# Performance work log

Hardware: AMD Instinct MI355X
Metric: run time of the kernel (lower is better)

## Reference

```python
import jax, jax.numpy as jnp
import numpy as np

B = 16
S_IN, S_DIM, Z_DIM, PE_DIM = 21, 256, 64, 64
REGIONS = ["cdr3", "pep", "mhc", "hv", "hj", "lv", "lj"]
LENS = {"cdr3": 24, "pep": 16, "mhc": 48, "hv": 104, "hj": 16, "lv": 104, "lj": 14}
L_TOTAL = 1 + sum(LENS.values())  # 327 = collapse token + all regions (full masks)
N_COND = 6


def _pos_enc(L):
    # sinusoidal PE matching one_d_positional_encoding: sin for even i, cos for odd i,
    # both with divisor 10000**(i/dim)
    pos = jnp.arange(L, dtype=jnp.float32)
    i = jnp.arange(PE_DIM)
    ang = pos[:, None] / (10000.0 ** (i.astype(jnp.float32) / PE_DIM))
    return jnp.where(i % 2 == 0, jnp.sin(ang), jnp.cos(ang))  # [L, 64]


def _pair_id():
    # region label per position: 0=psi, 1=cdr3, 2..7 = conditioning regions in order
    reg = np.concatenate([[0]] + [[k + 1] * LENS[r] for k, r in enumerate(REGIONS)])
    reg = jnp.asarray(reg, dtype=jnp.int32)
    ri, rj = reg[:, None], reg[None, :]
    i = jnp.arange(L_TOTAL, dtype=jnp.int32)[:, None]
    j = jnp.arange(L_TOTAL, dtype=jnp.int32)[None, :]
    p = jnp.zeros((L_TOTAL, L_TOTAL), dtype=jnp.int32)
    p = jnp.where((i == 0) | (j == 0), 1, p)                    # lvl1: psi <-> all
    p = jnp.where((i == 0) & (j == 0), 0, p)                    # lvl0: psi self
    cb = (ri == 1) & (rj == 1)
    p = jnp.where(cb & (jnp.abs(i - j) == 1), 2, p)             # lvl2: cdr3 sequential
    p = jnp.where(cb & (i != j) & (jnp.abs(i - j) != 1), 3, p)  # lvl3: cdr3 internal
    p = jnp.where(((ri == 1) & (rj >= 2)) | ((ri >= 2) & (rj == 1)), 4, p)  # lvl4
    p = jnp.where((ri >= 2) & (ri == rj), 5 + (ri - 2), p)      # lvl5..10: cond internal
    a = jnp.minimum(ri, rj) - 2
    b = jnp.maximum(ri, rj) - 2
    cross = a * (2 * N_COND - a - 1) // 2 + (b - a - 1)         # upper-tri pair index
    p = jnp.where((ri >= 2) & (rj >= 2) & (ri != rj), 11 + cross, p)  # lvl11..25
    return jnp.minimum(p, 31)


def _region_emb(seq, w2, seq_W, seq_b, pos_W, pos_b):
    # seq: [B, Lr, 21] -> [B, Lr, 256]
    se = jnp.einsum('bld,ed->ble', seq, seq_W) + seq_b
    pe = _pos_enc(seq.shape[1]) @ pos_W.T + pos_b  # [Lr, 256]
    return w2[0] * se + w2[1] * pe


def setup_inputs() -> dict:
    key = jax.random.key(0)
    ks = jax.random.split(key, 16)
    inp = {}
    for n, (name, r) in enumerate(zip(
            ['cdr3_xt', 'pep_seq', 'mhc_seq', 'hv_seq', 'hj_seq', 'lv_seq', 'lj_seq'], REGIONS)):
        inp[name] = jax.random.normal(ks[n], (B, LENS[r], S_IN), dtype=jnp.float32)
    inp['seq_W'] = jax.random.normal(ks[7], (S_DIM, S_IN), dtype=jnp.float32) * 0.1
    inp['seq_b'] = jnp.zeros((S_DIM,), dtype=jnp.float32)
    inp['pos_W'] = jax.random.normal(ks[8], (S_DIM, PE_DIM), dtype=jnp.float32) * 0.1
    inp['pos_b'] = jnp.zeros((S_DIM,), dtype=jnp.float32)
    inp['pair1_W'] = jax.random.normal(ks[9], (Z_DIM // 2, 8), dtype=jnp.float32) * 0.3
    inp['pair1_b'] = jnp.zeros((Z_DIM // 2,), dtype=jnp.float32)
    inp['pair2_W'] = jax.random.normal(ks[10], (Z_DIM // 2, 4), dtype=jnp.float32) * 0.3
    inp['pair2_b'] = jnp.zeros((Z_DIM // 2,), dtype=jnp.float32)
    inp['collapse_token'] = jax.random.normal(ks[11], (1, S_DIM), dtype=jnp.float32) * 0.1
    inp['collapse_weight'] = jnp.ones((1,), dtype=jnp.float32)
    inp['region_w'] = jax.random.uniform(ks[12], (7, 2), dtype=jnp.float32) + 0.5
    for name, r in zip(['cdr3_mask', 'pep_mask', 'mhc_mask', 'hv_mask', 'hj_mask', 'lv_mask', 'lj_mask'], REGIONS):
        inp[name] = jnp.ones((B, LENS[r]), dtype=jnp.int32)
    return inp


def reference(cdr3_xt, pep_seq, mhc_seq, hv_seq, hj_seq, lv_seq, lj_seq,
              seq_W, seq_b, pos_W, pos_b, pair1_W, pair1_b, pair2_W, pair2_b,
              collapse_token, collapse_weight, region_w,
              cdr3_mask, pep_mask, mhc_mask, hv_mask, hj_mask, lv_mask, lj_mask):
    # masks are all-ones -> every region is full-length (static shapes); they are
    # only used in torch to derive lengths, so they are closed-over constants here.
    seqs = [cdr3_xt, pep_seq, mhc_seq, hv_seq, hj_seq, lv_seq, lj_seq]
    parts = [jnp.broadcast_to(collapse_weight * collapse_token, (B, 1, S_DIM))]
    for k, seq in enumerate(seqs):
        parts.append(_region_emb(seq, region_w[k], seq_W, seq_b, pos_W, pos_b))
    s = jnp.concatenate(parts, axis=1)  # [B, 327, 256]
    p = _pair_id()                      # [327, 327] int32, identical across batch
    # one_hot(k, n) @ W.T + b  ==  (W.T + b)[k]  -> pure gather from tiny tables
    t1 = pair1_W.T + pair1_b            # [8, 32]
    t2 = pair2_W.T + pair2_b            # [4, 32]
    z = jnp.concatenate([t1[p // 4], t2[p % 4]], axis=-1)        # [327, 327, 64]
    z = jnp.broadcast_to(z[None], (B, L_TOTAL, L_TOTAL, Z_DIM))  # per-sample z list -> stacked
    return s, z
```

## Files before the change

kernel.cpp:

```cpp
#include <hip/hip_runtime.h>
#include <math.h>

#define NB 16
#define LTOT 327
#define SDIM 256
#define ZD 64

__device__ __constant__ int d_starts[7] = {1, 25, 41, 89, 193, 209, 313};
__device__ __constant__ int d_lens[7]   = {24, 16, 48, 104, 16, 104, 14};

__device__ __constant__ int seg_s[8] = {0, 1, 25, 41, 89, 193, 209, 313};
__device__ __constant__ int seg_e[8] = {1, 25, 41, 89, 193, 209, 313, 327};

__device__ __forceinline__ int regid(int x) {
    return (x >= 1) + (x >= 25) + (x >= 41) + (x >= 89) + (x >= 193) + (x >= 209) + (x >= 313);
}

__device__ __forceinline__ int pair_id(int i, int j, int ri, int rj) {
    if ((i == 0) && (j == 0)) return 0;
    if ((i == 0) || (j == 0)) return 1;
    if ((ri == 1) && (rj == 1)) {
        int d = i > j ? i - j : j - i;
        if (d == 1) return 2;
        if (d != 0) return 3;
        return 0;
    }
    if ((ri == 1) || (rj == 1)) return 4;
    if (ri == rj) return 5 + ri - 2;
    int a = (ri < rj ? ri : rj) - 2;
    int c = (ri < rj ? rj : ri) - 2;
    return 11 + a * (11 - a) / 2 + (c - a - 1);
}

__global__ __launch_bounds__(256) void pe_kernel(
    const float* __restrict__ posW, const float* __restrict__ posb,
    const float* __restrict__ rw, float* __restrict__ pe_full)
{
    int l = blockIdx.x;
    int e = threadIdx.x;
    __shared__ float sh_pe[64];

    int k = (l >= 25) + (l >= 41) + (l >= 89) + (l >= 193) + (l >= 209) + (l >= 313);
    int pl = (l == 0) ? 0 : (l - d_starts[k]);
    if (e < 64) {
        float scale = exp2f(-(float)e * (13.287712379549449f / 64.0f));
        float ang = (float)pl * scale;
        sh_pe[e] = (e & 1) ? cosf(ang) : sinf(ang);
    }
    __syncthreads();

    float pe = posb[e];
    const float* pwrow = posW + e * 64;
    #pragma unroll 8
    for (int i2 = 0; i2 < 64; i2++) pe = fmaf(sh_pe[i2], pwrow[i2], pe);
    pe_full[(size_t)l * SDIM + e] = rw[2 * k + 1] * pe;
}

__global__ __launch_bounds__(256) void s_kernel2(
    const float* __restrict__ s0, const float* __restrict__ s1,
    const float* __restrict__ s2, const float* __restrict__ s3,
    const float* __restrict__ s4, const float* __restrict__ s5,
    const float* __restrict__ s6,
    const float* __restrict__ seqW, const float* __restrict__ seqb,
    const float* __restrict__ ctok, const float* __restrict__ cw,
    const float* __restrict__ rw, const float* __restrict__ pe_full,
    float* __restrict__ out)
{
    int blk = blockIdx.x;
    int l = blk % LTOT;
    int b = blk / LTOT;
    int e = threadIdx.x;

    if (l == 0) {
        out[(size_t)blk * SDIM + e] = cw[0] * ctok[e];
        return;
    }
    __shared__ float sh_seq[21];
    int k = (l >= 25) + (l >= 41) + (l >= 89) + (l >= 193) + (l >= 209) + (l >= 313);
    int pl = l - d_starts[k];
    const float* sp;
    switch (k) {
        case 0: sp = s0; break; case 1: sp = s1; break; case 2: sp = s2; break;
        case 3: sp = s3; break; case 4: sp = s4; break; case 5: sp = s5; break;
        default: sp = s6;
    }
    if (e < 21) sh_seq[e] = sp[((size_t)b * d_lens[k] + pl) * 21 + e];
    __syncthreads();

    float se = seqb[e];
    const float* wrow = seqW + e * 21;
    #pragma unroll
    for (int d = 0; d < 21; d++) se = fmaf(sh_seq[d], wrow[d], se);

    out[(size_t)blk * SDIM + e] = rw[2 * k] * se + pe_full[(size_t)l * SDIM + e];
}

__global__ __launch_bounds__(256) void s_kernel(
    const float* __restrict__ s0, const float* __restrict__ s1,
    const float* __restrict__ s2, const float* __restrict__ s3,
    const float* __restrict__ s4, const float* __restrict__ s5,
    const float* __restrict__ s6,
    const float* __restrict__ seqW, const float* __restrict__ seqb,
    const float* __restrict__ posW, const float* __restrict__ posb,
    const float* __restrict__ ctok, const float* __restrict__ cw,
    const float* __restrict__ rw,
    float* __restrict__ out)
{
    int blk = blockIdx.x;
    int l = blk % LTOT;
    int b = blk / LTOT;
    int e = threadIdx.x;
    if (l == 0) { out[(size_t)blk * SDIM + e] = cw[0] * ctok[e]; return; }
    __shared__ float sh_seq[21];
    __shared__ float sh_pe[64];
    int k = (l >= 25) + (l >= 41) + (l >= 89) + (l >= 193) + (l >= 209) + (l >= 313);
    int pl = l - d_starts[k];
    const float* sp;
    switch (k) {
        case 0: sp = s0; break; case 1: sp = s1; break; case 2: sp = s2; break;
        case 3: sp = s3; break; case 4: sp = s4; break; case 5: sp = s5; break;
        default: sp = s6;
    }
    if (e < 21) sh_seq[e] = sp[((size_t)b * d_lens[k] + pl) * 21 + e];
    if (e < 64) {
        float scale = exp2f(-(float)e * (13.287712379549449f / 64.0f));
        float ang = (float)pl * scale;
        sh_pe[e] = (e & 1) ? cosf(ang) : sinf(ang);
    }
    __syncthreads();
    float se = seqb[e];
    const float* wrow = seqW + e * 21;
    #pragma unroll
    for (int d = 0; d < 21; d++) se = fmaf(sh_seq[d], wrow[d], se);
    float pe = posb[e];
    const float* pwrow = posW + e * 64;
    #pragma unroll 8
    for (int i2 = 0; i2 < 64; i2++) pe = fmaf(sh_pe[i2], pwrow[i2], pe);
    out[(size_t)blk * SDIM + e] = rw[2 * k] * se + rw[2 * k + 1] * pe;
}

#define TSTRIDE 68

__global__ __launch_bounds__(256) void z_kernel(
    const float* __restrict__ p1W, const float* __restrict__ p1b,
    const float* __restrict__ p2W, const float* __restrict__ p2b,
    float* __restrict__ outz)
{
    __shared__ __align__(16) float table[32 * TSTRIDE];
    int t = threadIdx.x;

    for (int idx = t; idx < 32 * 64; idx += 256) {
        int p = idx >> 6, c = idx & 63;
        float v;
        if (c < 32) v = p1W[c * 8 + (p >> 2)] + p1b[c];
        else        v = p2W[(c - 32) * 4 + (p & 3)] + p2b[c - 32];
        table[p * TSTRIDE + c] = v;
    }
    __syncthreads();

    int blk = blockIdx.x;
    int i = blk % LTOT;
    int ri = regid(i);
    int c4 = t & 15;
    int jo = t >> 4;

    float4* dst = (float4*)(outz + (size_t)blk * (LTOT * ZD));

    #pragma unroll
    for (int s = 0; s < 8; s++) {
        int js = seg_s[s], je = seg_e[s];
        if (ri == 1 && s == 1) {
            float4 v0 = *(const float4*)(table + 0 * TSTRIDE + c4 * 4);
            float4 v2 = *(const float4*)(table + 2 * TSTRIDE + c4 * 4);
            float4 v3 = *(const float4*)(table + 3 * TSTRIDE + c4 * 4);
            for (int j = js + jo; j < je; j += 16) {
                int d = i > j ? i - j : j - i;
                float4 v = (d == 0) ? v0 : ((d == 1) ? v2 : v3);
                dst[j * 16 + c4] = v;
            }
        } else {
            int p = pair_id(i, js, ri, regid(js));
            float4 v = *(const float4*)(table + p * TSTRIDE + c4 * 4);
            for (int j = js + jo; j < je; j += 16) {
                dst[j * 16 + c4] = v;
            }
        }
    }
}

extern "C" void kernel_launch(void* const* d_in, const int* in_sizes, int n_in,
                              void* d_out, int out_size, void* d_ws, size_t ws_size,
                              hipStream_t stream) {
    const float* seq0 = (const float*)d_in[0];
    const float* seq1 = (const float*)d_in[1];
    const float* seq2 = (const float*)d_in[2];
    const float* seq3 = (const float*)d_in[3];
    const float* seq4 = (const float*)d_in[4];
    const float* seq5 = (const float*)d_in[5];
    const float* seq6 = (const float*)d_in[6];
    const float* seqW = (const float*)d_in[7];
    const float* seqb = (const float*)d_in[8];
    const float* posW = (const float*)d_in[9];
    const float* posb = (const float*)d_in[10];
    const float* p1W  = (const float*)d_in[11];
    const float* p1b  = (const float*)d_in[12];
    const float* p2W  = (const float*)d_in[13];
    const float* p2b  = (const float*)d_in[14];
    const float* ctok = (const float*)d_in[15];
    const float* cw   = (const float*)d_in[16];
    const float* rw   = (const float*)d_in[17];

    float* out = (float*)d_out;
    float* outz = out + (size_t)NB * LTOT * SDIM;

    z_kernel<<<NB * LTOT, 256, 0, stream>>>(p1W, p1b, p2W, p2b, outz);

    if (ws_size >= (size_t)LTOT * SDIM * sizeof(float)) {
        float* pe_full = (float*)d_ws;
        pe_kernel<<<LTOT, 256, 0, stream>>>(posW, posb, rw, pe_full);
        s_kernel2<<<NB * LTOT, 256, 0, stream>>>(seq0, seq1, seq2, seq3, seq4, seq5, seq6,
                                                 seqW, seqb, ctok, cw, rw, pe_full, out);
    } else {
        s_kernel<<<NB * LTOT, 256, 0, stream>>>(seq0, seq1, seq2, seq3, seq4, seq5, seq6,
                                                seqW, seqb, posW, posb, ctok, cw, rw, out);
    }
}
```

Measured before the change: 507.1 us.

## Fuse z and s kernels into one launch with nontemporal 32-byte stores

Merges the z pair-table broadcast kernel and the s embedding kernel into one launch, with the block index choosing which branch runs. The z stores become nontemporal, and each thread writes two 16-byte vectors (32 bytes) per row. The s path now stages seqW in shared memory. The aim is to cut a launch, let the small s work overlap the bandwidth-bound z writes, and keep the z output from polluting cache. The cost is a larger shared allocation for every block, which may lower occupancy for the z blocks.

```diff
diff --git a/kernel.cpp b/kernel.cpp
--- a/kernel.cpp
+++ b/kernel.cpp
@@ -5,6 +5,9 @@
 #define LTOT 327
 #define SDIM 256
 #define ZD 64
+#define NZ (NB * LTOT)
+
+typedef float nt4 __attribute__((ext_vector_type(4)));
 
 __device__ __constant__ int d_starts[7] = {1, 25, 41, 89, 193, 209, 313};
 __device__ __constant__ int d_lens[7]   = {24, 16, 48, 104, 16, 104, 14};
@@ -56,7 +59,11 @@
     pe_full[(size_t)l * SDIM + e] = rw[2 * k + 1] * pe;
 }
 
-__global__ __launch_bounds__(256) void s_kernel2(
+#define TSTRIDE 68
+
+__global__ __launch_bounds__(256) void fused_zs(
+    const float* __restrict__ p1W, const float* __restrict__ p1b,
+    const float* __restrict__ p2W, const float* __restrict__ p2b,
     const float* __restrict__ s0, const float* __restrict__ s1,
     const float* __restrict__ s2, const float* __restrict__ s3,
     const float* __restrict__ s4, const float* __restrict__ s5,
@@ -64,82 +71,93 @@
     const float* __restrict__ seqW, const float* __restrict__ seqb,
     const float* __restrict__ ctok, const float* __restrict__ cw,
     const float* __restrict__ rw, const float* __restrict__ pe_full,
-    float* __restrict__ out)
-{
+    float* __restrict__ out, float* __restrict__ outz)
+{
+    __shared__ __align__(16) float smem[5408];
+    int t = threadIdx.x;
     int blk = blockIdx.x;
-    int l = blk % LTOT;
-    int b = blk / LTOT;
-    int e = threadIdx.x;
-
-    if (l == 0) {
-        out[(size_t)blk * SDIM + e] = cw[0] * ctok[e];
-        return;
-    }
-    __shared__ float sh_seq[21];
-    int k = (l >= 25) + (l >= 41) + (l >= 89) + (l >= 193) + (l >= 209) + (l >= 313);
-    int pl = l - d_starts[k];
-    const float* sp;
-    switch (k) {
-        case 0: sp = s0; break; case 1: sp = s1; break; case 2: sp = s2; break;
-        case 3: sp = s3; break; case 4: sp = s4; break; case 5: sp = s5; break;
-        default: sp = s6;
-    }
-    if (e < 21) sh_seq[e] = sp[((size_t)b * d_lens[k] + pl) * 21 + e];
-    __syncthreads();
-
-    float se = seqb[e];
-    const float* wrow = seqW + e * 21;
-    #pragma unroll
-    for (int d = 0; d < 21; d++) se = fmaf(sh_seq[d], wrow[d], se);
-
-    out[(size_t)blk * SDIM + e] = rw[2 * k] * se + pe_full[(size_t)l * SDIM + e];
-}
-
-__global__ __launch_bounds__(256) void s_kernel(
-    const float* __restrict__ s0, const float* __restrict__ s1,
-    const float* __restrict__ s2, const float* __restrict__ s3,
-    const float* __restrict__ s4, const float* __restrict__ s5,
-    const float* __restrict__ s6,
-    const float* __restrict__ seqW, const float* __restrict__ seqb,
-    const float* __restrict__ posW, const float* __restrict__ posb,
-    const float* __restrict__ ctok, const float* __restrict__ cw,
-    const float* __restrict__ rw,
-    float* __restrict__ out)
-{
-    int blk = blockIdx.x;
-    int l = blk % LTOT;
-    int b = blk / LTOT;
-    int e = threadIdx.x;
-    if (l == 0) { out[(size_t)blk * SDIM + e] = cw[0] * ctok[e]; return; }
-    __shared__ float sh_seq[21];
-    __shared__ float sh_pe[64];
-    int k = (l >= 25) + (l >= 41) + (l >= 89) + (l >= 193) + (l >= 209) + (l >= 313);
-    int pl = l - d_starts[k];
-    const float* sp;
-    switch (k) {
-        case 0: sp = s0; break; case 1: sp = s1; break; case 2: sp = s2; break;
-        case 3: sp = s3; break; case 4: sp = s4; break; case 5: sp = s5; break;
-        default: sp = s6;
-    }
-    if (e < 21) sh_seq[e] = sp[((size_t)b * d_lens[k] + pl) * 21 + e];
-    if (e < 64) {
-        float scale = exp2f(-(float)e * (13.287712379549449f / 64.0f));
-        float ang = (float)pl * scale;
-        sh_pe[e] = (e & 1) ? cosf(ang) : sinf(ang);
-    }
-    __syncthreads();
-    float se = seqb[e];
-    const float* wrow = seqW + e * 21;
-    #pragma unroll
-    for (int d = 0; d < 21; d++) se = fmaf(sh_seq[d], wrow[d], se);
-    float pe = posb[e];
-    const float* pwrow = posW + e * 64;
-    #pragma unroll 8
-    for (int i2 = 0; i2 < 64; i2++) pe = fmaf(sh_pe[i2], pwrow[i2], pe);
-    out[(size_t)blk * SDIM + e] = rw[2 * k] * se + rw[2 * k + 1] * pe;
-}
-
-#define TSTRIDE 68
+
+    if (blk < NZ) {
+        float* table = smem;
+        for (int idx = t; idx < 32 * 64; idx += 256) {
+            int p = idx >> 6, c = idx & 63;
+            float v;
+            if (c < 32) v = p1W[c * 8 + (p >> 2)] + p1b[c];
+            else        v = p2W[(c - 32) * 4 + (p & 3)] + p2b[c - 32];
+            table[p * TSTRIDE + c] = v;
+        }
+        __syncthreads();
+
+        int i = blk % LTOT;
+        int ri = regid(i);
+        int c8 = t & 7;
+        int jo = t >> 3;
+
+        nt4* dst = (nt4*)(outz + (size_t)blk * (LTOT * ZD)) + c8 * 2;
+
+        #pragma unroll
+        for (int s = 0; s < 8; s++) {
+            int js = seg_s[s], je = seg_e[s];
+            if (ri == 1 && s == 1) {
+                const nt4* r0 = (const nt4*)(table + 0 * TSTRIDE) + c8 * 2;
+                const nt4* r2 = (const nt4*)(table + 2 * TSTRIDE) + c8 * 2;
+                const nt4* r3 = (const nt4*)(table + 3 * TSTRIDE) + c8 * 2;
+                nt4 v0a = r0[0], v0b = r0[1];
+                nt4 v2a = r2[0], v2b = r2[1];
+                nt4 v3a = r3[0], v3b = r3[1];
+                for (int j = js + jo; j < je; j += 32) {
+                    int d = i > j ? i - j : j - i;
+                    nt4 va = (d == 0) ? v0a : ((d == 1) ? v2a : v3a);
+                    nt4 vb = (d == 0) ? v0b : ((d == 1) ? v2b : v3b);
+                    __builtin_nontemporal_store(va, dst + j * 16);
+                    __builtin_nontemporal_store(vb, dst + j * 16 + 1);
+                }
+            } else {
+                int p = pair_id(i, js, ri, regid(js));
+                const nt4* rp = (const nt4*)(table + p * TSTRIDE) + c8 * 2;
+                nt4 va = rp[0], vb = rp[1];
+                for (int j = js + jo; j < je; j += 32) {
+                    __builtin_nontemporal_store(va, dst + j * 16);
+                    __builtin_nontemporal_store(vb, dst + j * 16 + 1);
+                }
+            }
+        }
+    } else {
+        int sb = blk - NZ;
+        int l = sb % LTOT;
+        int b = sb / LTOT;
+        int e = t;
+
+        if (l == 0) {
+            out[(size_t)sb * SDIM + e] = cw[0] * ctok[e];
+            return;
+        }
+        float* sh_w   = smem;
+        float* sh_seq = smem + 5376;
+
+        const float4* wsrc = (const float4*)seqW;
+        float4* wdst = (float4*)sh_w;
+        for (int idx = t; idx < 1344; idx += 256) wdst[idx] = wsrc[idx];
+
+        int k = (l >= 25) + (l >= 41) + (l >= 89) + (l >= 193) + (l >= 209) + (l >= 313);
+        int pl = l - d_starts[k];
+        const float* sp;
+        switch (k) {
+            case 0: sp = s0; break; case 1: sp = s1; break; case 2: sp = s2; break;
+            case 3: sp = s3; break; case 4: sp = s4; break; case 5: sp = s5; break;
+            default: sp = s6;
+        }
+        if (e < 21) sh_seq[e] = sp[((size_t)b * d_lens[k] + pl) * 21 + e];
+        __syncthreads();
+
+        float se = seqb[e];
+        const float* wrow = sh_w + e * 21;
+        #pragma unroll
+        for (int d = 0; d < 21; d++) se = fmaf(sh_seq[d], wrow[d], se);
+
+        out[(size_t)sb * SDIM + e] = rw[2 * k] * se + pe_full[(size_t)l * SDIM + e];
+    }
+}
 
 __global__ __launch_bounds__(256) void z_kernel(
     const float* __restrict__ p1W, const float* __restrict__ p1b,
@@ -148,7 +166,6 @@
 {
     __shared__ __align__(16) float table[32 * TSTRIDE];
     int t = threadIdx.x;
-
     for (int idx = t; idx < 32 * 64; idx += 256) {
         int p = idx >> 6, c = idx & 63;
         float v;
@@ -163,7 +180,6 @@
     int ri = regid(i);
     int c4 = t & 15;
     int jo = t >> 4;
-
     float4* dst = (float4*)(outz + (size_t)blk * (LTOT * ZD));
 
     #pragma unroll
@@ -186,6 +202,50 @@
             }
         }
     }
+}
+
+__global__ __launch_bounds__(256) void s_kernel(
+    const float* __restrict__ s0, const float* __restrict__ s1,
+    const float* __restrict__ s2, const float* __restrict__ s3,
+    const float* __restrict__ s4, const float* __restrict__ s5,
+    const float* __restrict__ s6,
+    const float* __restrict__ seqW, const float* __restrict__ seqb,
+    const float* __restrict__ posW, const float* __restrict__ posb,
+    const float* __restrict__ ctok, const float* __restrict__ cw,
+    const float* __restrict__ rw,
+    float* __restrict__ out)
+{
+    int blk = blockIdx.x;
+    int l = blk % LTOT;
+    int b = blk / LTOT;
+    int e = threadIdx.x;
+    if (l == 0) { out[(size_t)blk * SDIM + e] = cw[0] * ctok[e]; return; }
+    __shared__ float sh_seq[21];
+    __shared__ float sh_pe[64];
+    int k = (l >= 25) + (l >= 41) + (l >= 89) + (l >= 193) + (l >= 209) + (l >= 313);
+    int pl = l - d_starts[k];
+    const float* sp;
+    switch (k) {
+        case 0: sp = s0; break; case 1: sp = s1; break; case 2: sp = s2; break;
+        case 3: sp = s3; break; case 4: sp = s4; break; case 5: sp = s5; break;
+        default: sp = s6;
+    }
+    if (e < 21) sh_seq[e] = sp[((size_t)b * d_lens[k] + pl) * 21 + e];
+    if (e < 64) {
+        float scale = exp2f(-(float)e * (13.287712379549449f / 64.0f));
+        float ang = (float)pl * scale;
+        sh_pe[e] = (e & 1) ? cosf(ang) : sinf(ang);
+    }
+    __syncthreads();
+    float se = seqb[e];
+    const float* wrow = seqW + e * 21;
+    #pragma unroll
+    for (int d = 0; d < 21; d++) se = fmaf(sh_seq[d], wrow[d], se);
+    float pe = posb[e];
+    const float* pwrow = posW + e * 64;
+    #pragma unroll 8
+    for (int i2 = 0; i2 < 64; i2++) pe = fmaf(sh_pe[i2], pwrow[i2], pe);
+    out[(size_t)blk * SDIM + e] = rw[2 * k] * se + rw[2 * k + 1] * pe;
 }
 
 extern "C" void kernel_launch(void* const* d_in, const int* in_sizes, int n_in,
@@ -213,15 +273,16 @@
     float* out = (float*)d_out;
     float* outz = out + (size_t)NB * LTOT * SDIM;
 
-    z_kernel<<<NB * LTOT, 256, 0, stream>>>(p1W, p1b, p2W, p2b, outz);
-
     if (ws_size >= (size_t)LTOT * SDIM * sizeof(float)) {
         float* pe_full = (float*)d_ws;
         pe_kernel<<<LTOT, 256, 0, stream>>>(posW, posb, rw, pe_full);
-        s_kernel2<<<NB * LTOT, 256, 0, stream>>>(seq0, seq1, seq2, seq3, seq4, seq5, seq6,
-                                                 seqW, seqb, ctok, cw, rw, pe_full, out);
+        fused_zs<<<2 * NZ, 256, 0, stream>>>(p1W, p1b, p2W, p2b,
+                                             seq0, seq1, seq2, seq3, seq4, seq5, seq6,
+                                             seqW, seqb, ctok, cw, rw, pe_full,
+                                             out, outz);
     } else {
-        s_kernel<<<NB * LTOT, 256, 0, stream>>>(seq0, seq1, seq2, seq3, seq4, seq5, seq6,
-                                                seqW, seqb, posW, posb, ctok, cw, rw, out);
-    }
-}
+        z_kernel<<<NZ, 256, 0, stream>>>(p1W, p1b, p2W, p2b, outz);
+        s_kernel<<<NZ, 256, 0, stream>>>(seq0, seq1, seq2, seq3, seq4, seq5, seq6,
+                                         seqW, seqb, posW, posb, ctok, cw, rw, out);
+    }
+}
```

Result: slower. 635.3 us (+25.3%).

## Fuse z and s kernels into one launch with interleaved block roles

Applied to the files above, without the earlier changes.

Replaces the three launches (z_kernel, pe_kernel, s_kernel2) with a single kernel. Even blocks fill the z pair table and odd blocks compute s embeddings, so the compute-light s work overlaps with the store-bound z writes. The precomputed positional-encoding workspace path is dropped, so each s block now recomputes the 64x256 positional projection itself. That adds redundant ALU work in exchange for removing launch gaps and serialization between kernels.

```diff
diff --git a/kernel.cpp b/kernel.cpp
--- a/kernel.cpp
+++ b/kernel.cpp
@@ -5,6 +5,8 @@
 #define LTOT 327
 #define SDIM 256
 #define ZD 64
+#define NZ (NB * LTOT)
+#define TSTRIDE 68
 
 __device__ __constant__ int d_starts[7] = {1, 25, 41, 89, 193, 209, 313};
 __device__ __constant__ int d_lens[7]   = {24, 16, 48, 104, 16, 104, 14};
@@ -32,70 +34,9 @@
     return 11 + a * (11 - a) / 2 + (c - a - 1);
 }
 
-__global__ __launch_bounds__(256) void pe_kernel(
-    const float* __restrict__ posW, const float* __restrict__ posb,
-    const float* __restrict__ rw, float* __restrict__ pe_full)
-{
-    int l = blockIdx.x;
-    int e = threadIdx.x;
-    __shared__ float sh_pe[64];
-
-    int k = (l >= 25) + (l >= 41) + (l >= 89) + (l >= 193) + (l >= 209) + (l >= 313);
-    int pl = (l == 0) ? 0 : (l - d_starts[k]);
-    if (e < 64) {
-        float scale = exp2f(-(float)e * (13.287712379549449f / 64.0f));
-        float ang = (float)pl * scale;
-        sh_pe[e] = (e & 1) ? cosf(ang) : sinf(ang);
-    }
-    __syncthreads();
-
-    float pe = posb[e];
-    const float* pwrow = posW + e * 64;
-    #pragma unroll 8
-    for (int i2 = 0; i2 < 64; i2++) pe = fmaf(sh_pe[i2], pwrow[i2], pe);
-    pe_full[(size_t)l * SDIM + e] = rw[2 * k + 1] * pe;
-}
-
-__global__ __launch_bounds__(256) void s_kernel2(
-    const float* __restrict__ s0, const float* __restrict__ s1,
-    const float* __restrict__ s2, const float* __restrict__ s3,
-    const float* __restrict__ s4, const float* __restrict__ s5,
-    const float* __restrict__ s6,
-    const float* __restrict__ seqW, const float* __restrict__ seqb,
-    const float* __restrict__ ctok, const float* __restrict__ cw,
-    const float* __restrict__ rw, const float* __restrict__ pe_full,
-    float* __restrict__ out)
-{
-    int blk = blockIdx.x;
-    int l = blk % LTOT;
-    int b = blk / LTOT;
-    int e = threadIdx.x;
-
-    if (l == 0) {
-        out[(size_t)blk * SDIM + e] = cw[0] * ctok[e];
-        return;
-    }
-    __shared__ float sh_seq[21];
-    int k = (l >= 25) + (l >= 41) + (l >= 89) + (l >= 193) + (l >= 209) + (l >= 313);
-    int pl = l - d_starts[k];
-    const float* sp;
-    switch (k) {
-        case 0: sp = s0; break; case 1: sp = s1; break; case 2: sp = s2; break;
-        case 3: sp = s3; break; case 4: sp = s4; break; case 5: sp = s5; break;
-        default: sp = s6;
-    }
-    if (e < 21) sh_seq[e] = sp[((size_t)b * d_lens[k] + pl) * 21 + e];
-    __syncthreads();
-
-    float se = seqb[e];
-    const float* wrow = seqW + e * 21;
-    #pragma unroll
-    for (int d = 0; d < 21; d++) se = fmaf(sh_seq[d], wrow[d], se);
-
-    out[(size_t)blk * SDIM + e] = rw[2 * k] * se + pe_full[(size_t)l * SDIM + e];
-}
-
-__global__ __launch_bounds__(256) void s_kernel(
+__global__ __launch_bounds__(256) void fused_all(
+    const float* __restrict__ p1W, const float* __restrict__ p1b,
+    const float* __restrict__ p2W, const float* __restrict__ p2b,
     const float* __restrict__ s0, const float* __restrict__ s1,
     const float* __restrict__ s2, const float* __restrict__ s3,
     const float* __restrict__ s4, const float* __restrict__ s5,
@@ -104,87 +45,91 @@
     const float* __restrict__ posW, const float* __restrict__ posb,
     const float* __restrict__ ctok, const float* __restrict__ cw,
     const float* __restrict__ rw,
-    float* __restrict__ out)
+    float* __restrict__ out, float* __restrict__ outz)
 {
-    int blk = blockIdx.x;
-    int l = blk % LTOT;
-    int b = blk / LTOT;
-    int e = threadIdx.x;
-    if (l == 0) { out[(size_t)blk * SDIM + e] = cw[0] * ctok[e]; return; }
-    __shared__ float sh_seq[21];
-    __shared__ float sh_pe[64];
-    int k = (l >= 25) + (l >= 41) + (l >= 89) + (l >= 193) + (l >= 209) + (l >= 313);
-    int pl = l - d_starts[k];
-    const float* sp;
-    switch (k) {
-        case 0: sp = s0; break; case 1: sp = s1; break; case 2: sp = s2; break;
-        case 3: sp = s3; break; case 4: sp = s4; break; case 5: sp = s5; break;
-        default: sp = s6;
-    }
-    if (e < 21) sh_seq[e] = sp[((size_t)b * d_lens[k] + pl) * 21 + e];
-    if (e < 64) {
-        float scale = exp2f(-(float)e * (13.287712379549449f / 64.0f));
-        float ang = (float)pl * scale;
-        sh_pe[e] = (e & 1) ? cosf(ang) : sinf(ang);
-    }
-    __syncthreads();
-    float se = seqb[e];
-    const float* wrow = seqW + e * 21;
-    #pragma unroll
-    for (int d = 0; d < 21; d++) se = fmaf(sh_seq[d], wrow[d], se);
-    float pe = posb[e];
-    const float* pwrow = posW + e * 64;
-    #pragma unroll 8
-    for (int i2 = 0; i2 < 64; i2++) pe = fmaf(sh_pe[i2], pwrow[i2], pe);
-    out[(size_t)blk * SDIM + e] = rw[2 * k] * se + rw[2 * k + 1] * pe;
-}
+    __shared__ __align__(16) float smem[32 * TSTRIDE];
+    int t = threadIdx.x;
+    int blk0 = blockIdx.x;
 
-#define TSTRIDE 68
+    if ((blk0 & 1) == 0) {
+        int blk = blk0 >> 1;
+        float* table = smem;
+        for (int idx = t; idx < 32 * 64; idx += 256) {
+            int p = idx >> 6, c = idx & 63;
+            float v;
+            if (c < 32) v = p1W[c * 8 + (p >> 2)] + p1b[c];
+            else        v = p2W[(c - 32) * 4 + (p & 3)] + p2b[c - 32];
+            table[p * TSTRIDE + c] = v;
+        }
+        __syncthreads();
 
-__global__ __launch_bounds__(256) void z_kernel(
-    const float* __restrict__ p1W, const float* __restrict__ p1b,
-    const float* __restrict__ p2W, const float* __restrict__ p2b,
-    float* __restrict__ outz)
-{
-    __shared__ __align__(16) float table[32 * TSTRIDE];
-    int t = threadIdx.x;
+        int i = blk % LTOT;
+        int ri = regid(i);
+        int c4 = t & 15;
+        int jo = t >> 4;
 
-    for (int idx = t; idx < 32 * 64; idx += 256) {
-        int p = idx >> 6, c = idx & 63;
-        float v;
-        if (c < 32) v = p1W[c * 8 + (p >> 2)] + p1b[c];
-        else        v = p2W[(c - 32) * 4 + (p & 3)] + p2b[c - 32];
-        table[p * TSTRIDE + c] = v;
-    }
-    __syncthreads();
+        float4* dst = (float4*)(outz + (size_t)blk * (LTOT * ZD));
 
-    int blk = blockIdx.x;
-    int i = blk % LTOT;
-    int ri = regid(i);
-    int c4 = t & 15;
-    int jo = t >> 4;
-
-    float4* dst = (float4*)(outz + (size_t)blk * (LTOT * ZD));
-
-    #pragma unroll
-    for (int s = 0; s < 8; s++) {
-        int js = seg_s[s], je = seg_e[s];
-        if (ri == 1 && s == 1) {
-            float4 v0 = *(const float4*)(table + 0 * TSTRIDE + c4 * 4);
-            float4 v2 = *(const float4*)(table + 2 * TSTRIDE + c4 * 4);
-            float4 v3 = *(const float4*)(table + 3 * TSTRIDE + c4 * 4);
-            for (int j = js + jo; j < je; j += 16) {
-                int d = i > j ? i - j : j - i;
-                float4 v = (d == 0) ? v0 : ((d == 1) ? v2 : v3);
-                dst[j * 16 + c4] = v;
-            }
-        } else {
-            int p = pair_id(i, js, ri, regid(js));
-            float4 v = *(const float4*)(table + p * TSTRIDE + c4 * 4);
-            for (int j = js + jo; j < je; j += 16) {
-                dst[j * 16 + c4] = v;
+        #pragma unroll
+        for (int s = 0; s < 8; s++) {
+            int js = seg_s[s], je = seg_e[s];
+            if (ri == 1 && s == 1) {
+                float4 v0 = *(const float4*)(table + 0 * TSTRIDE + c4 * 4);
+                float4 v2 = *(const float4*)(table + 2 * TSTRIDE + c4 * 4);
+                float4 v3 = *(const float4*)(table + 3 * TSTRIDE + c4 * 4);
+                for (int j = js + jo; j < je; j += 16) {
+                    int d = i > j ? i - j : j - i;
+                    float4 v = (d == 0) ? v0 : ((d == 1) ? v2 : v3);
+                    dst[j * 16 + c4] = v;
+                }
+            } else {
+                int p = pair_id(i, js, ri, regid(js));
+                float4 v = *(const float4*)(table + p * TSTRIDE + c4 * 4);
+                for (int j = js + jo; j < je; j += 16) {
+                    dst[j * 16 + c4] = v;
+                }
             }
         }
+    } else {
+        int sb = blk0 >> 1;
+        int l = sb % LTOT;
+        int b = sb / LTOT;
+        int e = t;
+
+        if (l == 0) {
+            out[(size_t)sb * SDIM + e] = cw[0] * ctok[e];
+            return;
+        }
+        float* sh_seq = smem;
+        float* sh_pe  = smem + 32;
+
+        int k = (l >= 25) + (l >= 41) + (l >= 89) + (l >= 193) + (l >= 209) + (l >= 313);
+        int pl = l - d_starts[k];
+        const float* sp;
+        switch (k) {
+            case 0: sp = s0; break; case 1: sp = s1; break; case 2: sp = s2; break;
+            case 3: sp = s3; break; case 4: sp = s4; break; case 5: sp = s5; break;
+            default: sp = s6;
+        }
+        if (e < 21) sh_seq[e] = sp[((size_t)b * d_lens[k] + pl) * 21 + e];
+        if (e < 64) {
+            float scale = exp2f(-(float)e * (13.287712379549449f / 64.0f));
+            float ang = (float)pl * scale;
+            sh_pe[e] = (e & 1) ? cosf(ang) : sinf(ang);
+        }
+        __syncthreads();
+
+        float se = seqb[e];
+        const float* wrow = seqW + e * 21;
+        #pragma unroll
+        for (int d = 0; d < 21; d++) se = fmaf(sh_seq[d], wrow[d], se);
+
+        float pe = posb[e];
+        const float* pwrow = posW + e * 64;
+        #pragma unroll 8
+        for (int i2 = 0; i2 < 64; i2++) pe = fmaf(sh_pe[i2], pwrow[i2], pe);
+
+        out[(size_t)sb * SDIM + e] = rw[2 * k] * se + rw[2 * k + 1] * pe;
     }
 }
 
@@ -213,15 +158,8 @@
     float* out = (float*)d_out;
     float* outz = out + (size_t)NB * LTOT * SDIM;
 
-    z_kernel<<<NB * LTOT, 256, 0, stream>>>(p1W, p1b, p2W, p2b, outz);
-
-    if (ws_size >= (size_t)LTOT * SDIM * sizeof(float)) {
-        float* pe_full = (float*)d_ws;
-        pe_kernel<<<LTOT, 256, 0, stream>>>(posW, posb, rw, pe_full);
-        s_kernel2<<<NB * LTOT, 256, 0, stream>>>(seq0, seq1, seq2, seq3, seq4, seq5, seq6,
-                                                 seqW, seqb, ctok, cw, rw, pe_full, out);
-    } else {
-        s_kernel<<<NB * LTOT, 256, 0, stream>>>(seq0, seq1, seq2, seq3, seq4, seq5, seq6,
-                                                seqW, seqb, posW, posb, ctok, cw, rw, out);
-    }
+    fused_all<<<2 * NZ, 256, 0, stream>>>(p1W, p1b, p2W, p2b,
+                                          seq0, seq1, seq2, seq3, seq4, seq5, seq6,
+                                          seqW, seqb, posW, posb, ctok, cw, rw,
+                                          out, outz);
 }
```

Result: no change. 510.3 us (+0.6%).
